# Kernel tuning notes

Hardware: AMD Instinct MI355X
Metric: run time of the kernel (lower is better)

## Reference

```python
import jax, jax.numpy as jnp
import numpy as np

H = 2048       # hidden_size
NH = 16        # num query heads
NKV = 4        # num key/value heads
HD = 128       # head_dim
EPS = 1e-6
ROPE_BASE = 10000.0


def rms_norm(x, w):
    xf = x.astype(jnp.float32)
    var = jnp.mean(xf * xf, axis=-1, keepdims=True)
    return (w * (xf * jax.lax.rsqrt(var + EPS)).astype(x.dtype))


def rope_cos_sin(seq_len, dtype):
    inv_freq = 1.0 / (ROPE_BASE ** (jnp.arange(0, HD, 2, dtype=jnp.float32) / HD))
    pos = jnp.arange(seq_len, dtype=jnp.float32)
    ang = pos[:, None] * inv_freq[None, :]            # [S, HD/2]
    emb = jnp.concatenate([ang, ang], axis=-1)        # [S, HD]
    return jnp.cos(emb).astype(dtype), jnp.sin(emb).astype(dtype)


def rotate_half(x):
    x1, x2 = jnp.split(x, 2, axis=-1)
    return jnp.concatenate([-x2, x1], axis=-1)


def setup_inputs() -> dict:
    key = jax.random.key(0)
    ks = jax.random.split(key, 8)
    B, S = 2, 2048
    hidden_states = jax.random.normal(ks[0], (B, S, H), dtype=jnp.float32)
    # additive causal mask [B,1,S,S]
    causal = jnp.where(jnp.tril(jnp.ones((S, S), dtype=bool)), 0.0, -1e9).astype(jnp.float32)
    attention_mask = jnp.broadcast_to(causal[None, None], (B, 1, S, S))
    sc = 1.0 / np.sqrt(H)
    Wq = jax.random.normal(ks[1], (NH * HD, H), dtype=jnp.float32) * sc
    Wk = jax.random.normal(ks[2], (NKV * HD, H), dtype=jnp.float32) * sc
    Wv = jax.random.normal(ks[3], (NKV * HD, H), dtype=jnp.float32) * sc
    Wo = jax.random.normal(ks[4], (H, NH * HD), dtype=jnp.float32) * sc
    q_norm_w = jnp.ones((HD,), dtype=jnp.float32)
    k_norm_w = jnp.ones((HD,), dtype=jnp.float32)
    return {"hidden_states": hidden_states, "attention_mask": attention_mask,
            "Wq": Wq, "Wk": Wk, "Wv": Wv, "Wo": Wo,
            "q_norm_w": q_norm_w, "k_norm_w": k_norm_w}


def reference(hidden_states, attention_mask, Wq, Wk, Wv, Wo, q_norm_w, k_norm_w):
    B, S, _ = hidden_states.shape
    # projections (nn.Linear: x @ W.T)
    q = (hidden_states @ Wq.T).reshape(B, S, NH, HD).transpose(0, 2, 1, 3)   # [B,NH,S,HD]
    k = (hidden_states @ Wk.T).reshape(B, S, NKV, HD).transpose(0, 2, 1, 3)  # [B,NKV,S,HD]
    v = (hidden_states @ Wv.T).reshape(B, S, NKV, HD).transpose(0, 2, 1, 3)
    # QK RMSNorm over head_dim
    q = rms_norm(q, q_norm_w)
    k = rms_norm(k, k_norm_w)
    # RoPE
    cos, sin = rope_cos_sin(S, q.dtype)        # [S,HD]
    q = q * cos + rotate_half(q) * sin
    k = k * cos + rotate_half(k) * sin
    # GQA: repeat kv heads
    n_rep = NH // NKV
    k = jnp.repeat(k, n_rep, axis=1)           # [B,NH,S,HD]
    v = jnp.repeat(v, n_rep, axis=1)
    # attention
    scores = jnp.einsum('bhqd,bhkd->bhqk', q, k) / np.sqrt(HD)
    scores = scores + attention_mask
    probs = jax.nn.softmax(scores, axis=-1)
    attn = jnp.einsum('bhqk,bhkd->bhqd', probs, v)
    attn = attn.transpose(0, 2, 1, 3).reshape(B, S, NH * HD)
    return attn @ Wo.T
```

## Files before the change

### kernel.cpp

```cpp
#include <hip/hip_runtime.h>
#include <hip/hip_bf16.h>
#include <math.h>

#define NH 16
#define NKV 4
#define HD 128
#define SEQ 2048
#define BATCH 2
#define EPSF 1e-6f
#define QKV 3072

typedef __attribute__((ext_vector_type(8))) short bf16x8;
typedef __attribute__((ext_vector_type(4))) short short4v;
typedef __attribute__((ext_vector_type(4))) float f32x4;

__device__ __forceinline__ short f2bf(float x) {
    unsigned u = __float_as_uint(x);
    u += 0x7fffu + ((u >> 16) & 1u);
    return (short)(u >> 16);
}
__device__ __forceinline__ float bf2f(short x) {
    return __uint_as_float((unsigned)(unsigned short)x << 16);
}
__device__ __forceinline__ unsigned pkbf(float a, float b) {
    __hip_bfloat162 h = __float22bfloat162_rn(float2{a, b});
    unsigned r; __builtin_memcpy(&r, &h, 4); return r;
}

__device__ __forceinline__ void gll16(const short* g, short* l) {
    __builtin_amdgcn_global_load_lds(
        (const __attribute__((address_space(1))) unsigned*)g,
        (__attribute__((address_space(3))) unsigned*)l, 16, 0, 0);
}

__global__ __launch_bounds__(256)
void cast_all(const float* __restrict__ hs, const float* __restrict__ Wq,
              const float* __restrict__ Wk, const float* __restrict__ Wv,
              const float* __restrict__ Wo, short* __restrict__ hsb,
              short* __restrict__ wqkv, short* __restrict__ wob)
{
    const size_t MEG = 1024 * 1024;
    const int id = blockIdx.x;
    const float* s;
    short* d;
    size_t off;
    if (id < 8192)       { s = hs; d = hsb;            off = (size_t)id * 1024; }
    else if (id < 12288) { s = Wq; d = wqkv;           off = (size_t)(id - 8192) * 1024; }
    else if (id < 13312) { s = Wk; d = wqkv + 4 * MEG; off = (size_t)(id - 12288) * 1024; }
    else if (id < 14336) { s = Wv; d = wqkv + 5 * MEG; off = (size_t)(id - 13312) * 1024; }
    else                 { s = Wo; d = wob;            off = (size_t)(id - 14336) * 1024; }
    const size_t i = off + threadIdx.x * 4;
    float4 v = *(const float4*)(s + i);
    short4v o;
    o.x = f2bf(v.x); o.y = f2bf(v.y); o.z = f2bf(v.z); o.w = f2bf(v.w);
    *(short4v*)(d + i) = o;
}

template<bool OUT_BF16>
__global__ __launch_bounds__(256, 3)
void gemm_nt_mfma(const short* __restrict__ A, const short* __restrict__ B,
                  void* __restrict__ Cv, int N, int K, int gridX, int total)
{
    __shared__ short As[128 * 64];
    __shared__ short Bs[128 * 64];

    const int tid = threadIdx.x;
    const int w = tid >> 6, lane = tid & 63;
    const int quad = lane >> 4, ln = lane & 15;
    const int mw = (w >> 1) * 64, nw = (w & 1) * 64;

    const int id = blockIdx.x;
    const int t = (id & 7) * (total >> 3) + (id >> 3);
    const int n0 = (t % gridX) * 128;
    const int m0 = (t / gridX) * 128;

    const int rr = lane >> 3;
    const int gsw = ((lane & 7) ^ rr) * 8;
    const short* Ag[4]; const short* Bg[4];
    short* Al[4]; short* Bl[4];
    #pragma unroll
    for (int r = 0; r < 4; ++r) {
        const int row = w * 8 + 32 * r + rr;
        Ag[r] = A + (size_t)(m0 + row) * K + gsw;
        Bg[r] = B + (size_t)(n0 + row) * K + gsw;
        Al[r] = &As[(w * 8 + 32 * r) * 64];
        Bl[r] = &Bs[(w * 8 + 32 * r) * 64];
    }

    const int col0 = ((quad) ^ (ln & 7)) * 8;
    const int col1 = ((4 + quad) ^ (ln & 7)) * 8;

    f32x4 acc[4][4];
    #pragma unroll
    for (int i = 0; i < 4; ++i)
        #pragma unroll
        for (int j = 0; j < 4; ++j)
            acc[i][j] = (f32x4){0.f, 0.f, 0.f, 0.f};

    for (int k0 = 0; k0 < K; k0 += 64) {
        __syncthreads();
        #pragma unroll
        for (int r = 0; r < 4; ++r) {
            gll16(Ag[r] + k0, Al[r]);
            gll16(Bg[r] + k0, Bl[r]);
        }
        __syncthreads();

        #pragma unroll
        for (int ks = 0; ks < 2; ++ks) {
            const int col = ks ? col1 : col0;
            bf16x8 af[4], bfr[4];
            #pragma unroll
            for (int i = 0; i < 4; ++i)
                af[i] = *(const bf16x8*)&As[(mw + i * 16 + ln) * 64 + col];
            #pragma unroll
            for (int j = 0; j < 4; ++j)
                bfr[j] = *(const bf16x8*)&Bs[(nw + j * 16 + ln) * 64 + col];
            #pragma unroll
            for (int i = 0; i < 4; ++i)
                #pragma unroll
                for (int j = 0; j < 4; ++j)
                    acc[i][j] = __builtin_amdgcn_mfma_f32_16x16x32_bf16(
                        af[i], bfr[j], acc[i][j], 0, 0, 0);
        }
    }

    #pragma unroll
    for (int i = 0; i < 4; ++i) {
        #pragma unroll
        for (int reg = 0; reg < 4; ++reg) {
            const int row = m0 + mw + i * 16 + quad * 4 + reg;
            const size_t base = (size_t)row * N + n0 + nw;
            #pragma unroll
            for (int j = 0; j < 4; ++j) {
                if (OUT_BF16)
                    ((short*)Cv)[base + j * 16 + ln] = f2bf(acc[i][j][reg]);
                else
                    ((float*)Cv)[base + j * 16 + ln] = acc[i][j][reg];
            }
        }
    }
}

__global__ __launch_bounds__(256)
void norm_rope_bf16(short* __restrict__ qkv, const float* __restrict__ qw,
                    const float* __restrict__ kw)
{
    const int wave = threadIdx.x >> 6;
    const int lane = threadIdx.x & 63;
    const long vec = (long)blockIdx.x * 4 + wave;
    const long NQ = (long)BATCH * SEQ * NH;

    short* base;
    const float* w;
    int s;
    if (vec < NQ) {
        const long token = vec / NH;
        const int h = (int)(vec % NH);
        s = (int)(token % SEQ);
        base = qkv + token * QKV + h * HD;
        w = qw;
    } else {
        const long t = vec - NQ;
        const long token = t / NKV;
        const int kvh = (int)(t % NKV);
        s = (int)(token % SEQ);
        base = qkv + token * QKV + 2048 + kvh * HD;
        w = kw;
    }

    float x0 = bf2f(base[lane]);
    float x1 = bf2f(base[lane + 64]);
    float ss = x0 * x0 + x1 * x1;
    #pragma unroll
    for (int off = 32; off; off >>= 1) ss += __shfl_xor(ss, off, 64);
    const float r = rsqrtf(ss * (1.0f / HD) + EPSF);
    x0 = x0 * r * w[lane];
    x1 = x1 * r * w[lane + 64];

    const float inv_freq = expf(-(float)lane * (logf(10000.0f) / 64.0f));
    const float ang = (float)s * inv_freq;
    const float c = cosf(ang);
    const float sn = sinf(ang);
    base[lane]      = f2bf(x0 * c - x1 * sn);
    base[lane + 64] = f2bf(x1 * c + x0 * sn);
}

__global__ __launch_bounds__(256)
void transpose_v(const short* __restrict__ qkv, short* __restrict__ vT)
{
    __shared__ short T[32][33];
    const int bx = blockIdx.x;
    const int st = bx & 63;
    const int dt = (bx >> 6) & 3;
    const int bk = bx >> 8;
    const int s0 = st * 32, d0 = dt * 32;
    const int tid = threadIdx.x;
    const long tok0 = (long)(bk >> 2) * SEQ + s0;
    const int kvh = bk & 3;

    const int rs = tid >> 3;
    const int rc = (tid & 7) * 4;
    short4v val = *(const short4v*)(qkv + (tok0 + rs) * QKV + 2560 + kvh * HD + d0 + rc);
    T[rc + 0][rs] = val.x; T[rc + 1][rs] = val.y;
    T[rc + 2][rs] = val.z; T[rc + 3][rs] = val.w;
    __syncthreads();

    const int wd = tid >> 3;
    const int wsc = (tid & 7) * 4;
    short4v ov;
    ov.x = T[wd][wsc + 0]; ov.y = T[wd][wsc + 1];
    ov.z = T[wd][wsc + 2]; ov.w = T[wd][wsc + 3];
    *(short4v*)(vT + ((size_t)bk * HD + d0 + wd) * SEQ + s0 + wsc) = ov;
}

__global__ __launch_bounds__(512, 4)
void flash_attn_mfma(const short* __restrict__ qkv, const short* __restrict__ vT,
                     short* __restrict__ o)
{
    __shared__ short Ks[64 * 128];
    __shared__ short Vt[128 * 64];
    __shared__ short Ps[8][16 * 64];

    const int tid = threadIdx.x;
    const int w = tid >> 6;
    const int lane = tid & 63;
    const int quad = lane >> 4;
    const int ln = lane & 15;
    const int lnm = ln & 7;
    const int side = w >> 2;
    const int sw = w & 3;

    const int bx = blockIdx.x;
    const int pair = bx & 15;
    const int bh = bx >> 4;
    const int h = bh & 15;
    const int b = bh >> 4;
    const int kvh = h >> 2;
    const int qa = pair, qb = 31 - pair;
    const int qX = side ? qb : qa;
    const int rX = qX * 64 + sw * 16;

    const float SC = 0.08838834764831845f * 1.4426950408889634f;

    int colK[4];
    #pragma unroll
    for (int f = 0; f < 4; ++f) {
        const int lg = f * 4 + quad;
        colK[f] = ((lg & 8) | ((lg ^ lnm) & 7)) * 8;
    }
    const int colA = (quad ^ lnm) * 8;
    const int colB = ((4 + quad) ^ lnm) * 8;

    bf16x8 qf[4];
    {
        const short* qrow = qkv + (size_t)(b * SEQ + rX + ln) * QKV + h * HD;
        #pragma unroll
        for (int f = 0; f < 4; ++f)
            qf[f] = *(const bf16x8*)(qrow + f * 32 + quad * 8);
    }

    f32x4 Oa[8];
    #pragma unroll
    for (int dg = 0; dg < 8; ++dg) Oa[dg] = (f32x4){0.f, 0.f, 0.f, 0.f};
    float mX = -1e30f, lX = 0.f;

    const short* kbase = qkv + (size_t)(b * SEQ) * QKV + 2048 + kvh * HD;
    const short* vbase = vT + (size_t)(b * NKV + kvh) * HD * SEQ;

    bf16x8 kp[2], vp[2];
    auto prefetch = [&](int k0) {
        #pragma unroll
        for (int i = 0; i < 2; ++i) {
            const int e = tid + i * 512;
            kp[i] = *(const bf16x8*)(kbase + (size_t)(k0 + (e >> 4)) * QKV + (e & 15) * 8);
            vp[i] = *(const bf16x8*)(vbase + (size_t)(e >> 3) * SEQ + k0 + (e & 7) * 8);
        }
    };
    prefetch(0);

    for (int kt = 0; kt <= qb; ++kt) {
        const int k0 = kt * 64;
        __syncthreads();
        #pragma unroll
        for (int i = 0; i < 2; ++i) {
            const int e = tid + i * 512;
            const int kr = e >> 4, kg = e & 15;
            *(bf16x8*)&Ks[kr * 128 + ((kg & 8) | ((kg ^ (kr & 7)) & 7)) * 8] = kp[i];
            const int vd = e >> 3, vg = e & 7;
            *(bf16x8*)&Vt[vd * 64 + ((vg ^ (vd & 7)) * 8)] = vp[i];
        }
        __syncthreads();
        if (kt < qb) prefetch(k0 + 64);

        if (kt <= qX) {
            f32x4 s[4];
            __builtin_amdgcn_s_setprio(1);
            #pragma unroll
            for (int g = 0; g < 4; ++g) {
                f32x4 acc = (f32x4){0.f, 0.f, 0.f, 0.f};
                #pragma unroll
                for (int f = 0; f < 4; ++f) {
                    bf16x8 kf = *(const bf16x8*)&Ks[(g * 16 + ln) * 128 + colK[f]];
                    acc = __builtin_amdgcn_mfma_f32_16x16x32_bf16(kf, qf[f], acc, 0, 0, 0);
                }
                s[g] = acc;
            }
            __builtin_amdgcn_s_setprio(0);
            if (kt == qX) {
                const int qrow = rX + ln;
                #pragma unroll
                for (int g = 0; g < 4; ++g)
                    #pragma unroll
                    for (int reg = 0; reg < 4; ++reg) {
                        const int key = k0 + g * 16 + quad * 4 + reg;
                        if (key > qrow) s[g][reg] = -1e30f;
                    }
            }
            float mt = s[0][0];
            #pragma unroll
            for (int g = 0; g < 4; ++g)
                #pragma unroll
                for (int reg = 0; reg < 4; ++reg)
                    mt = fmaxf(mt, s[g][reg]);
            mt = fmaxf(mt, __shfl_xor(mt, 16, 64));
            mt = fmaxf(mt, __shfl_xor(mt, 32, 64));
            const float mnew = fmaxf(mX, mt);
            const bool defer = __all((mnew - mX) * SC <= 6.0f);
            const float mref = defer ? mX : mnew;
            const float c1 = SC * mref;
            const float alpha = exp2f(__builtin_fmaf(SC, mX, -c1));
            float ps = 0.f;
            #pragma unroll
            for (int g = 0; g < 4; ++g) {
                float p0 = exp2f(__builtin_fmaf(s[g][0], SC, -c1));
                float p1 = exp2f(__builtin_fmaf(s[g][1], SC, -c1));
                float p2 = exp2f(__builtin_fmaf(s[g][2], SC, -c1));
                float p3 = exp2f(__builtin_fmaf(s[g][3], SC, -c1));
                ps += (p0 + p1) + (p2 + p3);
                uint2 pk;
                pk.x = pkbf(p0, p1);
                pk.y = pkbf(p2, p3);
                const int sg = (2 * g + (quad >> 1)) ^ lnm;
                *(uint2*)&Ps[w][ln * 64 + sg * 8 + (quad & 1) * 4] = pk;
            }
            ps += __shfl_xor(ps, 16, 64);
            ps += __shfl_xor(ps, 32, 64);
            mX = mref;
            if (defer) {
                lX += ps;
            } else {
                lX = lX * alpha + ps;
                #pragma unroll
                for (int dg = 0; dg < 8; ++dg) {
                    Oa[dg][0] *= alpha; Oa[dg][1] *= alpha;
                    Oa[dg][2] *= alpha; Oa[dg][3] *= alpha;
                }
            }
            __asm volatile("s_waitcnt lgkmcnt(0)" ::: "memory");
            bf16x8 pf0 = *(const bf16x8*)&Ps[w][ln * 64 + colA];
            bf16x8 pf1 = *(const bf16x8*)&Ps[w][ln * 64 + colB];
            __builtin_amdgcn_s_setprio(1);
            #pragma unroll
            for (int dg = 0; dg < 8; ++dg) {
                bf16x8 vf0 = *(const bf16x8*)&Vt[(dg * 16 + ln) * 64 + colA];
                bf16x8 vf1 = *(const bf16x8*)&Vt[(dg * 16 + ln) * 64 + colB];
                Oa[dg] = __builtin_amdgcn_mfma_f32_16x16x32_bf16(vf0, pf0, Oa[dg], 0, 0, 0);
                Oa[dg] = __builtin_amdgcn_mfma_f32_16x16x32_bf16(vf1, pf1, Oa[dg], 0, 0, 0);
            }
            __builtin_amdgcn_s_setprio(0);
        }
    }

    {
        const float inv = 1.0f / lX;
        short* orow = o + ((size_t)(b * SEQ + rX + ln) * NH + h) * HD;
        #pragma unroll
        for (int dg = 0; dg < 8; ++dg) {
            uint2 ov;
            ov.x = pkbf(Oa[dg][0] * inv, Oa[dg][1] * inv);
            ov.y = pkbf(Oa[dg][2] * inv, Oa[dg][3] * inv);
            *(uint2*)(orow + dg * 16 + quad * 4) = ov;
        }
    }
}

extern "C" void kernel_launch(void* const* d_in, const int* in_sizes, int n_in,
                              void* d_out, int out_size, void* d_ws, size_t ws_size,
                              hipStream_t stream)
{
    const float* hs = (const float*)d_in[0];
    const float* Wq = (const float*)d_in[2];
    const float* Wk = (const float*)d_in[3];
    const float* Wv = (const float*)d_in[4];
    const float* Wo = (const float*)d_in[5];
    const float* qw = (const float*)d_in[6];
    const float* kw = (const float*)d_in[7];
    float* out = (float*)d_out;

    const size_t MEG = 1024 * 1024;
    short* hsb  = (short*)d_ws;
    short* wqkv = hsb + 8 * MEG;
    short* wob  = wqkv + 6 * MEG;
    short* qkvb = wob + 4 * MEG;
    short* vT   = (short*)d_out;

    dim3 blk(256);

    cast_all<<<dim3(18432), blk, 0, stream>>>(hs, Wq, Wk, Wv, Wo, hsb, wqkv, wob);

    gemm_nt_mfma<true><<<dim3(768), blk, 0, stream>>>(
        hsb, wqkv, qkvb, QKV, 2048, 24, 768);

    norm_rope_bf16<<<dim3((BATCH * SEQ * (NH + NKV)) / 4), blk, 0, stream>>>(
        qkvb, qw, kw);

    transpose_v<<<dim3(2048), blk, 0, stream>>>(qkvb, vT);

    flash_attn_mfma<<<dim3(512), dim3(512), 0, stream>>>(qkvb, vT, hsb);

    gemm_nt_mfma<false><<<dim3(512), blk, 0, stream>>>(
        hsb, wob, out, 2048, 2048, 16, 512);
}
```

Baseline: 327.1 us.

## Replace 128x128 GEMM with double-buffered 256x256 tile, 8-wave pipelined kernel

```diff
diff --git a/kernel.cpp b/kernel.cpp
--- a/kernel.cpp
+++ b/kernel.cpp
@@ -56,87 +56,140 @@
     *(short4v*)(d + i) = o;
 }
 
+#define GPHASE(mh, nh, ISSUE)                                                  \
+  {                                                                            \
+    const short* Ab = &As[cb][0];                                              \
+    const short* Bb = &Bs[cb][0];                                              \
+    bf16x8 af[4][2], bfr[2][2];                                                \
+    _Pragma("unroll")                                                          \
+    for (int i = 0; i < 4; ++i) {                                              \
+      const int ar = (wm * 128 + (mh) * 64 + i * 16 + ln) * 64;                \
+      af[i][0] = *(const bf16x8*)&Ab[ar + colA];                               \
+      af[i][1] = *(const bf16x8*)&Ab[ar + colB];                               \
+    }                                                                          \
+    _Pragma("unroll")                                                          \
+    for (int j = 0; j < 2; ++j) {                                              \
+      const int br = (wn * 64 + (nh) * 32 + j * 16 + ln) * 64;                 \
+      bfr[j][0] = *(const bf16x8*)&Bb[br + colA];                              \
+      bfr[j][1] = *(const bf16x8*)&Bb[br + colB];                              \
+    }                                                                          \
+    ISSUE;                                                                     \
+    __builtin_amdgcn_s_barrier();                                              \
+    __asm volatile("s_waitcnt lgkmcnt(0)" ::: "memory");                       \
+    __builtin_amdgcn_sched_barrier(0);                                         \
+    __builtin_amdgcn_s_setprio(1);                                             \
+    _Pragma("unroll")                                                          \
+    for (int i = 0; i < 4; ++i)                                                \
+      _Pragma("unroll")                                                        \
+      for (int j = 0; j < 2; ++j) {                                            \
+        acc[(mh) * 4 + i][(nh) * 2 + j] =                                      \
+            __builtin_amdgcn_mfma_f32_16x16x32_bf16(                           \
+                af[i][0], bfr[j][0], acc[(mh) * 4 + i][(nh) * 2 + j], 0, 0, 0);\
+        acc[(mh) * 4 + i][(nh) * 2 + j] =                                      \
+            __builtin_amdgcn_mfma_f32_16x16x32_bf16(                           \
+                af[i][1], bfr[j][1], acc[(mh) * 4 + i][(nh) * 2 + j], 0, 0, 0);\
+      }                                                                        \
+    __builtin_amdgcn_s_setprio(0);                                             \
+    __builtin_amdgcn_s_barrier();                                              \
+  }
+
 template<bool OUT_BF16>
-__global__ __launch_bounds__(256, 3)
-void gemm_nt_mfma(const short* __restrict__ A, const short* __restrict__ B,
-                  void* __restrict__ Cv, int N, int K, int gridX, int total)
-{
-    __shared__ short As[128 * 64];
-    __shared__ short Bs[128 * 64];
+__global__ __launch_bounds__(512, 2)
+void gemm_nt_256(const short* __restrict__ A, const short* __restrict__ B,
+                 void* __restrict__ Cv, int N, int K, int gridX, int total)
+{
+    __shared__ short As[2][256 * 64];
+    __shared__ short Bs[2][256 * 64];
 
     const int tid = threadIdx.x;
     const int w = tid >> 6, lane = tid & 63;
     const int quad = lane >> 4, ln = lane & 15;
-    const int mw = (w >> 1) * 64, nw = (w & 1) * 64;
+    const int lnm = ln & 7;
+    const int wm = w >> 2, wn = w & 3;
 
     const int id = blockIdx.x;
-    const int t = (id & 7) * (total >> 3) + (id >> 3);
-    const int n0 = (t % gridX) * 128;
-    const int m0 = (t / gridX) * 128;
-
-    const int rr = lane >> 3;
-    const int gsw = ((lane & 7) ^ rr) * 8;
-    const short* Ag[4]; const short* Bg[4];
-    short* Al[4]; short* Bl[4];
+    const int tt = (id & 7) * (total >> 3) + (id >> 3);
+    const int n0 = (tt % gridX) * 256;
+    const int m0 = (tt / gridX) * 256;
+
+    const int T = K >> 6;
+    const int rr8 = lane >> 3, g8 = lane & 7;
+    const int gsw8 = ((g8 ^ rr8) * 8);
+
+    auto stage = [&](short* dst, int lrow, const short* src, int grow, int k0) {
+        gll16(src + (size_t)(grow + rr8) * K + k0 + gsw8, dst + lrow * 64);
+    };
+    auto issueAX = [&](int t) {
+        if (t >= T) return;
+        short* d = &As[t & 1][0]; const int k0 = t * 64;
+        stage(d, w * 8,       A, m0 + w * 8,       k0);
+        stage(d, 128 + w * 8, A, m0 + 128 + w * 8, k0);
+    };
+    auto issueAY = [&](int t) {
+        if (t >= T) return;
+        short* d = &As[t & 1][0]; const int k0 = t * 64;
+        stage(d, 64 + w * 8,  A, m0 + 64 + w * 8,  k0);
+        stage(d, 192 + w * 8, A, m0 + 192 + w * 8, k0);
+    };
+    auto issueBeven = [&](int t) {
+        if (t >= T) return;
+        short* d = &Bs[t & 1][0]; const int k0 = t * 64;
+        const int r0 = (w >> 2) * 64 + (w & 3) * 8;
+        stage(d, r0,       B, n0 + r0,       k0);
+        stage(d, 128 + r0, B, n0 + 128 + r0, k0);
+    };
+    auto issueBodd = [&](int t) {
+        if (t >= T) return;
+        short* d = &Bs[t & 1][0]; const int k0 = t * 64;
+        const int r0 = 32 + (w >> 2) * 64 + (w & 3) * 8;
+        stage(d, r0,       B, n0 + r0,       k0);
+        stage(d, 128 + r0, B, n0 + 128 + r0, k0);
+    };
+
+    const int colA = (quad ^ lnm) * 8;
+    const int colB = ((4 + quad) ^ lnm) * 8;
+
+    f32x4 acc[8][4];
     #pragma unroll
-    for (int r = 0; r < 4; ++r) {
-        const int row = w * 8 + 32 * r + rr;
-        Ag[r] = A + (size_t)(m0 + row) * K + gsw;
-        Bg[r] = B + (size_t)(n0 + row) * K + gsw;
-        Al[r] = &As[(w * 8 + 32 * r) * 64];
-        Bl[r] = &Bs[(w * 8 + 32 * r) * 64];
-    }
-
-    const int col0 = ((quad) ^ (ln & 7)) * 8;
-    const int col1 = ((4 + quad) ^ (ln & 7)) * 8;
-
-    f32x4 acc[4][4];
-    #pragma unroll
-    for (int i = 0; i < 4; ++i)
+    for (int i = 0; i < 8; ++i)
         #pragma unroll
         for (int j = 0; j < 4; ++j)
             acc[i][j] = (f32x4){0.f, 0.f, 0.f, 0.f};
 
-    for (int k0 = 0; k0 < K; k0 += 64) {
-        __syncthreads();
-        #pragma unroll
-        for (int r = 0; r < 4; ++r) {
-            gll16(Ag[r] + k0, Al[r]);
-            gll16(Bg[r] + k0, Bl[r]);
-        }
-        __syncthreads();
-
-        #pragma unroll
-        for (int ks = 0; ks < 2; ++ks) {
-            const int col = ks ? col1 : col0;
-            bf16x8 af[4], bfr[4];
+    issueAX(0); issueBeven(0); issueAY(0); issueBodd(0);
+    issueBeven(1); issueAX(1);
+    __asm volatile("s_waitcnt vmcnt(4)" ::: "memory");
+    __builtin_amdgcn_s_barrier();
+
+    for (int t = 0; t < T; ++t) {
+        const int cb = t & 1;
+        GPHASE(0, 0, issueAY(t + 1));
+        GPHASE(1, 0, issueBodd(t + 1));
+        GPHASE(0, 1, issueBeven(t + 2));
+        GPHASE(1, 1, {
+            issueAX(t + 2);
+            if (t + 2 < T) {
+                __asm volatile("s_waitcnt vmcnt(4)" ::: "memory");
+            } else {
+                __asm volatile("s_waitcnt vmcnt(0)" ::: "memory");
+            }
+        });
+    }
+
+    #pragma unroll
+    for (int mi = 0; mi < 8; ++mi) {
+        #pragma unroll
+        for (int reg = 0; reg < 4; ++reg) {
+            const int row = m0 + wm * 128 + (mi >> 2) * 64 + (mi & 3) * 16
+                          + quad * 4 + reg;
+            const size_t base = (size_t)row * N + n0 + wn * 64;
             #pragma unroll
-            for (int i = 0; i < 4; ++i)
-                af[i] = *(const bf16x8*)&As[(mw + i * 16 + ln) * 64 + col];
-            #pragma unroll
-            for (int j = 0; j < 4; ++j)
-                bfr[j] = *(const bf16x8*)&Bs[(nw + j * 16 + ln) * 64 + col];
-            #pragma unroll
-            for (int i = 0; i < 4; ++i)
-                #pragma unroll
-                for (int j = 0; j < 4; ++j)
-                    acc[i][j] = __builtin_amdgcn_mfma_f32_16x16x32_bf16(
-                        af[i], bfr[j], acc[i][j], 0, 0, 0);
-        }
-    }
-
-    #pragma unroll
-    for (int i = 0; i < 4; ++i) {
-        #pragma unroll
-        for (int reg = 0; reg < 4; ++reg) {
-            const int row = m0 + mw + i * 16 + quad * 4 + reg;
-            const size_t base = (size_t)row * N + n0 + nw;
-            #pragma unroll
-            for (int j = 0; j < 4; ++j) {
+            for (int nj = 0; nj < 4; ++nj) {
+                const int col = (nj >> 1) * 32 + (nj & 1) * 16 + ln;
                 if (OUT_BF16)
-                    ((short*)Cv)[base + j * 16 + ln] = f2bf(acc[i][j][reg]);
+                    ((short*)Cv)[base + col] = f2bf(acc[mi][nj][reg]);
                 else
-                    ((float*)Cv)[base + j * 16 + ln] = acc[i][j][reg];
+                    ((float*)Cv)[base + col] = acc[mi][nj][reg];
             }
         }
     }
@@ -409,8 +462,8 @@
 
     cast_all<<<dim3(18432), blk, 0, stream>>>(hs, Wq, Wk, Wv, Wo, hsb, wqkv, wob);
 
-    gemm_nt_mfma<true><<<dim3(768), blk, 0, stream>>>(
-        hsb, wqkv, qkvb, QKV, 2048, 24, 768);
+    gemm_nt_256<true><<<dim3(192), dim3(512), 0, stream>>>(
+        hsb, wqkv, qkvb, QKV, 2048, 12, 192);
 
     norm_rope_bf16<<<dim3((BATCH * SEQ * (NH + NKV)) / 4), blk, 0, stream>>>(
         qkvb, qw, kw);
@@ -419,6 +472,6 @@
 
     flash_attn_mfma<<<dim3(512), dim3(512), 0, stream>>>(qkvb, vT, hsb);
 
-    gemm_nt_mfma<false><<<dim3(512), blk, 0, stream>>>(
-        hsb, wob, out, 2048, 2048, 16, 512);
-}
+    gemm_nt_256<false><<<dim3(128), dim3(512), 0, stream>>>(
+        hsb, wob, out, 2048, 2048, 8, 128);
+}
```

Result: slower. 362.6 us (+10.8%).

## Split paired-tile attention blocks into single query tiles with interleaved heavy/light ordering

Applied to the files above, without the earlier changes.

```diff
diff --git a/kernel.cpp b/kernel.cpp
--- a/kernel.cpp
+++ b/kernel.cpp
@@ -214,13 +214,13 @@
     *(short4v*)(vT + ((size_t)bk * HD + d0 + wd) * SEQ + s0 + wsc) = ov;
 }
 
-__global__ __launch_bounds__(512, 4)
+__global__ __launch_bounds__(256, 4)
 void flash_attn_mfma(const short* __restrict__ qkv, const short* __restrict__ vT,
                      short* __restrict__ o)
 {
     __shared__ short Ks[64 * 128];
     __shared__ short Vt[128 * 64];
-    __shared__ short Ps[8][16 * 64];
+    __shared__ short Ps[4][16 * 64];
 
     const int tid = threadIdx.x;
     const int w = tid >> 6;
@@ -228,18 +228,15 @@
     const int quad = lane >> 4;
     const int ln = lane & 15;
     const int lnm = ln & 7;
-    const int side = w >> 2;
-    const int sw = w & 3;
 
     const int bx = blockIdx.x;
-    const int pair = bx & 15;
-    const int bh = bx >> 4;
+    const int j = bx >> 5;
+    const int g = (j & 1) ? (31 - (j >> 1)) : (j >> 1);
+    const int bh = bx & 31;
     const int h = bh & 15;
     const int b = bh >> 4;
     const int kvh = h >> 2;
-    const int qa = pair, qb = 31 - pair;
-    const int qX = side ? qb : qa;
-    const int rX = qX * 64 + sw * 16;
+    const int rX = g * 64 + w * 16;
 
     const float SC = 0.08838834764831845f * 1.4426950408889634f;
 
@@ -268,108 +265,106 @@
     const short* kbase = qkv + (size_t)(b * SEQ) * QKV + 2048 + kvh * HD;
     const short* vbase = vT + (size_t)(b * NKV + kvh) * HD * SEQ;
 
-    bf16x8 kp[2], vp[2];
+    bf16x8 kp[4], vp[4];
     auto prefetch = [&](int k0) {
         #pragma unroll
-        for (int i = 0; i < 2; ++i) {
-            const int e = tid + i * 512;
+        for (int i = 0; i < 4; ++i) {
+            const int e = tid + i * 256;
             kp[i] = *(const bf16x8*)(kbase + (size_t)(k0 + (e >> 4)) * QKV + (e & 15) * 8);
             vp[i] = *(const bf16x8*)(vbase + (size_t)(e >> 3) * SEQ + k0 + (e & 7) * 8);
         }
     };
     prefetch(0);
 
-    for (int kt = 0; kt <= qb; ++kt) {
+    for (int kt = 0; kt <= g; ++kt) {
         const int k0 = kt * 64;
         __syncthreads();
         #pragma unroll
-        for (int i = 0; i < 2; ++i) {
-            const int e = tid + i * 512;
+        for (int i = 0; i < 4; ++i) {
+            const int e = tid + i * 256;
             const int kr = e >> 4, kg = e & 15;
             *(bf16x8*)&Ks[kr * 128 + ((kg & 8) | ((kg ^ (kr & 7)) & 7)) * 8] = kp[i];
             const int vd = e >> 3, vg = e & 7;
             *(bf16x8*)&Vt[vd * 64 + ((vg ^ (vd & 7)) * 8)] = vp[i];
         }
         __syncthreads();
-        if (kt < qb) prefetch(k0 + 64);
-
-        if (kt <= qX) {
-            f32x4 s[4];
-            __builtin_amdgcn_s_setprio(1);
-            #pragma unroll
-            for (int g = 0; g < 4; ++g) {
-                f32x4 acc = (f32x4){0.f, 0.f, 0.f, 0.f};
+        if (kt < g) prefetch(k0 + 64);
+
+        f32x4 s[4];
+        __builtin_amdgcn_s_setprio(1);
+        #pragma unroll
+        for (int gi = 0; gi < 4; ++gi) {
+            f32x4 acc = (f32x4){0.f, 0.f, 0.f, 0.f};
+            #pragma unroll
+            for (int f = 0; f < 4; ++f) {
+                bf16x8 kf = *(const bf16x8*)&Ks[(gi * 16 + ln) * 128 + colK[f]];
+                acc = __builtin_amdgcn_mfma_f32_16x16x32_bf16(kf, qf[f], acc, 0, 0, 0);
+            }
+            s[gi] = acc;
+        }
+        __builtin_amdgcn_s_setprio(0);
+        if (kt == g) {
+            const int qrow = rX + ln;
+            #pragma unroll
+            for (int gi = 0; gi < 4; ++gi)
                 #pragma unroll
-                for (int f = 0; f < 4; ++f) {
-                    bf16x8 kf = *(const bf16x8*)&Ks[(g * 16 + ln) * 128 + colK[f]];
-                    acc = __builtin_amdgcn_mfma_f32_16x16x32_bf16(kf, qf[f], acc, 0, 0, 0);
+                for (int reg = 0; reg < 4; ++reg) {
+                    const int key = k0 + gi * 16 + quad * 4 + reg;
+                    if (key > qrow) s[gi][reg] = -1e30f;
                 }
-                s[g] = acc;
+        }
+        float mt = s[0][0];
+        #pragma unroll
+        for (int gi = 0; gi < 4; ++gi)
+            #pragma unroll
+            for (int reg = 0; reg < 4; ++reg)
+                mt = fmaxf(mt, s[gi][reg]);
+        mt = fmaxf(mt, __shfl_xor(mt, 16, 64));
+        mt = fmaxf(mt, __shfl_xor(mt, 32, 64));
+        const float mnew = fmaxf(mX, mt);
+        const bool defer = __all((mnew - mX) * SC <= 6.0f);
+        const float mref = defer ? mX : mnew;
+        const float c1 = SC * mref;
+        const float alpha = exp2f(__builtin_fmaf(SC, mX, -c1));
+        float ps = 0.f;
+        #pragma unroll
+        for (int gi = 0; gi < 4; ++gi) {
+            float p0 = exp2f(__builtin_fmaf(s[gi][0], SC, -c1));
+            float p1 = exp2f(__builtin_fmaf(s[gi][1], SC, -c1));
+            float p2 = exp2f(__builtin_fmaf(s[gi][2], SC, -c1));
+            float p3 = exp2f(__builtin_fmaf(s[gi][3], SC, -c1));
+            ps += (p0 + p1) + (p2 + p3);
+            uint2 pk;
+            pk.x = pkbf(p0, p1);
+            pk.y = pkbf(p2, p3);
+            const int sg = (2 * gi + (quad >> 1)) ^ lnm;
+            *(uint2*)&Ps[w][ln * 64 + sg * 8 + (quad & 1) * 4] = pk;
+        }
+        ps += __shfl_xor(ps, 16, 64);
+        ps += __shfl_xor(ps, 32, 64);
+        mX = mref;
+        if (defer) {
+            lX += ps;
+        } else {
+            lX = lX * alpha + ps;
+            #pragma unroll
+            for (int dg = 0; dg < 8; ++dg) {
+                Oa[dg][0] *= alpha; Oa[dg][1] *= alpha;
+                Oa[dg][2] *= alpha; Oa[dg][3] *= alpha;
             }
-            __builtin_amdgcn_s_setprio(0);
-            if (kt == qX) {
-                const int qrow = rX + ln;
-                #pragma unroll
-                for (int g = 0; g < 4; ++g)
-                    #pragma unroll
-                    for (int reg = 0; reg < 4; ++reg) {
-                        const int key = k0 + g * 16 + quad * 4 + reg;
-                        if (key > qrow) s[g][reg] = -1e30f;
-                    }
-            }
-            float mt = s[0][0];
-            #pragma unroll
-            for (int g = 0; g < 4; ++g)
-                #pragma unroll
-                for (int reg = 0; reg < 4; ++reg)
-                    mt = fmaxf(mt, s[g][reg]);
-            mt = fmaxf(mt, __shfl_xor(mt, 16, 64));
-            mt = fmaxf(mt, __shfl_xor(mt, 32, 64));
-            const float mnew = fmaxf(mX, mt);
-            const bool defer = __all((mnew - mX) * SC <= 6.0f);
-            const float mref = defer ? mX : mnew;
-            const float c1 = SC * mref;
-            const float alpha = exp2f(__builtin_fmaf(SC, mX, -c1));
-            float ps = 0.f;
-            #pragma unroll
-            for (int g = 0; g < 4; ++g) {
-                float p0 = exp2f(__builtin_fmaf(s[g][0], SC, -c1));
-                float p1 = exp2f(__builtin_fmaf(s[g][1], SC, -c1));
-                float p2 = exp2f(__builtin_fmaf(s[g][2], SC, -c1));
-                float p3 = exp2f(__builtin_fmaf(s[g][3], SC, -c1));
-                ps += (p0 + p1) + (p2 + p3);
-                uint2 pk;
-                pk.x = pkbf(p0, p1);
-                pk.y = pkbf(p2, p3);
-                const int sg = (2 * g + (quad >> 1)) ^ lnm;
-                *(uint2*)&Ps[w][ln * 64 + sg * 8 + (quad & 1) * 4] = pk;
-            }
-            ps += __shfl_xor(ps, 16, 64);
-            ps += __shfl_xor(ps, 32, 64);
-            mX = mref;
-            if (defer) {
-                lX += ps;
-            } else {
-                lX = lX * alpha + ps;
-                #pragma unroll
-                for (int dg = 0; dg < 8; ++dg) {
-                    Oa[dg][0] *= alpha; Oa[dg][1] *= alpha;
-                    Oa[dg][2] *= alpha; Oa[dg][3] *= alpha;
-                }
-            }
-            __asm volatile("s_waitcnt lgkmcnt(0)" ::: "memory");
-            bf16x8 pf0 = *(const bf16x8*)&Ps[w][ln * 64 + colA];
-            bf16x8 pf1 = *(const bf16x8*)&Ps[w][ln * 64 + colB];
-            __builtin_amdgcn_s_setprio(1);
-            #pragma unroll
-            for (int dg = 0; dg < 8; ++dg) {
-                bf16x8 vf0 = *(const bf16x8*)&Vt[(dg * 16 + ln) * 64 + colA];
-                bf16x8 vf1 = *(const bf16x8*)&Vt[(dg * 16 + ln) * 64 + colB];
-                Oa[dg] = __builtin_amdgcn_mfma_f32_16x16x32_bf16(vf0, pf0, Oa[dg], 0, 0, 0);
-                Oa[dg] = __builtin_amdgcn_mfma_f32_16x16x32_bf16(vf1, pf1, Oa[dg], 0, 0, 0);
-            }
-            __builtin_amdgcn_s_setprio(0);
-        }
+        }
+        __asm volatile("s_waitcnt lgkmcnt(0)" ::: "memory");
+        bf16x8 pf0 = *(const bf16x8*)&Ps[w][ln * 64 + colA];
+        bf16x8 pf1 = *(const bf16x8*)&Ps[w][ln * 64 + colB];
+        __builtin_amdgcn_s_setprio(1);
+        #pragma unroll
+        for (int dg = 0; dg < 8; ++dg) {
+            bf16x8 vf0 = *(const bf16x8*)&Vt[(dg * 16 + ln) * 64 + colA];
+            bf16x8 vf1 = *(const bf16x8*)&Vt[(dg * 16 + ln) * 64 + colB];
+            Oa[dg] = __builtin_amdgcn_mfma_f32_16x16x32_bf16(vf0, pf0, Oa[dg], 0, 0, 0);
+            Oa[dg] = __builtin_amdgcn_mfma_f32_16x16x32_bf16(vf1, pf1, Oa[dg], 0, 0, 0);
+        }
+        __builtin_amdgcn_s_setprio(0);
     }
 
     {
@@ -417,7 +412,7 @@
 
     transpose_v<<<dim3(2048), blk, 0, stream>>>(qkvb, vT);
 
-    flash_attn_mfma<<<dim3(512), dim3(512), 0, stream>>>(qkvb, vT, hsb);
+    flash_attn_mfma<<<dim3(1024), dim3(256), 0, stream>>>(qkvb, vT, hsb);
 
     gemm_nt_mfma<false><<<dim3(512), blk, 0, stream>>>(
         hsb, wob, out, 2048, 2048, 16, 512);
```

After: 406.9 us. +24.4%, slower.
